# Optimization experiments

Measured on AMD Instinct MI355X. Metric: run time of the kernel, lower is better.

Reference implementation:

```python
import jax, jax.numpy as jnp
import numpy as np

N_USERS = 100_000
N_ITEMS = 200_000
EMBED_DIM = 64
N_LAYERS = 2
AVG_DEG = 32
BATCH = 8192


def setup_inputs() -> dict:
    rng = np.random.default_rng(0)
    n_inter = N_USERS * AVG_DEG
    u = rng.integers(0, N_USERS, n_inter).astype(np.int32)
    i = rng.integers(0, N_ITEMS, n_inter).astype(np.int32)
    # symmetric bipartite adjacency: (u, n_users+i) and (n_users+i, u)
    rows = np.concatenate([u, i + N_USERS]).astype(np.int32)
    cols = np.concatenate([i + N_USERS, u]).astype(np.int32)
    n_nodes = N_USERS + N_ITEMS
    deg = np.bincount(rows, minlength=n_nodes).astype(np.float32)
    d_inv = np.where(deg > 0, deg ** -0.5, 0.0).astype(np.float32)
    vals = (d_inv[rows] * d_inv[cols]).astype(np.float32)  # D^-1/2 A D^-1/2

    key = jax.random.key(0)
    k1, k2, k3, k4 = jax.random.split(key, 4)
    return {
        "users": jax.random.randint(k1, (BATCH,), 0, N_USERS, dtype=jnp.int32),
        "items": jax.random.randint(k2, (BATCH,), 0, N_ITEMS, dtype=jnp.int32),
        "user_emb": 0.1 * jax.random.normal(k3, (N_USERS, EMBED_DIM), dtype=jnp.float32),
        "item_emb": 0.1 * jax.random.normal(k4, (N_ITEMS, EMBED_DIM), dtype=jnp.float32),
        "rows": jnp.asarray(rows),
        "cols": jnp.asarray(cols),
        "vals": jnp.asarray(vals),
    }


def reference(users, items, user_emb, item_emb, rows, cols, vals):
    n_users = user_emb.shape[0]
    n_nodes = n_users + item_emb.shape[0]
    all_emb = jnp.concatenate([user_emb, item_emb], axis=0)  # [N, D]
    emb = all_emb
    acc = all_emb  # running sum over layer outputs (fused mean)
    for _ in range(N_LAYERS):
        # SpMM: out[r] += vals_e * emb[cols_e] for each edge e with row r
        emb = jax.ops.segment_sum(vals[:, None] * emb[cols], rows,
                                  num_segments=n_nodes)
        acc = acc + emb
    light_out = acc / jnp.float32(N_LAYERS + 1)  # mean over stacked layers
    users_emb = light_out[users]                    # [B, D]
    items_emb = light_out[n_users + items]          # [B, D]
    scores = jnp.sum(users_emb * items_emb, axis=1)  # [B]
    return users_emb, items_emb, scores
```

## Files before the change

### kernel.cpp

```cpp
#include <hip/hip_runtime.h>
#include <hip/hip_bf16.h>


#define DIM 64
#define BSH 8
#define BN 256
#define NBMAX 1184
#define T_PAIRS 6144
#define T_STAGE 12288
#define K3_THREADS 512
#define SCAP 10240

__global__ void build_bb(const int* __restrict__ users,
                         const int* __restrict__ items,
                         unsigned char* __restrict__ bb,
                         unsigned char* __restrict__ flag,
                         int batch, int n_users) {
    int t = blockIdx.x * blockDim.x + threadIdx.x;
    if (t >= 2 * batch) return;
    int node = (t < batch) ? users[t] : (n_users + items[t - batch]);
    bb[node] = 1;
    flag[node] = 1;
}

__global__ void count_reserve(const int* __restrict__ rows,
                              const int* __restrict__ cols,
                              int n_pairs, int nb,
                              int* __restrict__ gcnt,
                              int* __restrict__ rcnt, int* __restrict__ rbase) {
    __shared__ int cnt[NBMAX];
    int t = threadIdx.x;
    for (int b = t; b < nb; b += blockDim.x) cnt[b] = 0;
    __syncthreads();
    int e0 = blockIdx.x * T_PAIRS;
    int e1 = min(e0 + T_PAIRS, n_pairs);
    int n = e1 - e0;
    int n4 = n >> 2;
    const int4* r4 = (const int4*)(rows + e0);
    const int4* c4 = (const int4*)(cols + e0);
    for (int j = t; j < n4; j += blockDim.x) {
        int4 r = r4[j];
        int4 c = c4[j];
        atomicAdd(&cnt[r.x >> BSH], 1); atomicAdd(&cnt[c.x >> BSH], 1);
        atomicAdd(&cnt[r.y >> BSH], 1); atomicAdd(&cnt[c.y >> BSH], 1);
        atomicAdd(&cnt[r.z >> BSH], 1); atomicAdd(&cnt[c.z >> BSH], 1);
        atomicAdd(&cnt[r.w >> BSH], 1); atomicAdd(&cnt[c.w >> BSH], 1);
    }
    for (int i = e0 + (n4 << 2) + t; i < e1; i += blockDim.x) {
        atomicAdd(&cnt[rows[i] >> BSH], 1);
        atomicAdd(&cnt[cols[i] >> BSH], 1);
    }
    __syncthreads();
    size_t rbo = (size_t)blockIdx.x * nb;
    for (int b = t; b < nb; b += blockDim.x) {
        int v = cnt[b];
        rcnt[rbo + b] = v;
        rbase[rbo + b] = v ? atomicAdd(&gcnt[b], v) : 0;
    }
}

__global__ void scan_buckets(const int* __restrict__ gcnt, int* __restrict__ gbase,
                             int* __restrict__ offs, int nb, int n_nodes) {
    __shared__ int s[NBMAX + 1];
    int t = threadIdx.x;
    for (int b = t; b < nb; b += blockDim.x) s[b] = gcnt[b];
    __syncthreads();
    if (t == 0) {
        int run = 0;
        for (int b = 0; b < nb; ++b) { int v = s[b]; s[b] = run; run += v; }
        s[nb] = run;
    }
    __syncthreads();
    for (int b = t; b <= nb; b += blockDim.x) gbase[b] = s[b];
    if (t == 0) offs[n_nodes] = s[nb];
}

__global__ __launch_bounds__(K3_THREADS)
void tile_scatter(const int* __restrict__ rows, const int* __restrict__ cols,
                  const int* __restrict__ rcnt, const int* __restrict__ rbase,
                  const int* __restrict__ gbase, unsigned* __restrict__ barr,
                  int n_pairs, int nb) {
    __shared__ unsigned stage[T_STAGE];
    __shared__ int loff[NBMAX + 1];
    __shared__ int cur[NBMAX];
    __shared__ int rb2[NBMAX];
    __shared__ int wsum[8];
    int t = threadIdx.x;
    int lane = t & 63, wave = t >> 6;
    size_t rbo = (size_t)blockIdx.x * nb;

    int lo = t * 3;
    int c0 = (lo     < nb) ? rcnt[rbo + lo]     : 0;
    int c1 = (lo + 1 < nb) ? rcnt[rbo + lo + 1] : 0;
    int c2 = (lo + 2 < nb) ? rcnt[rbo + lo + 2] : 0;
    int s = c0 + c1 + c2;
    int x = s;
    #pragma unroll
    for (int o = 1; o < 64; o <<= 1) { int y = __shfl_up(x, o); if (lane >= o) x += y; }
    if (lane == 63) wsum[wave] = x;
    __syncthreads();
    int wb = 0;
    #pragma unroll
    for (int w = 0; w < 8; ++w) if (w < wave) wb += wsum[w];
    int run = wb + (x - s);
    if (lo < nb) {
        loff[lo] = run; cur[lo] = run;
        rb2[lo] = gbase[lo] + rbase[rbo + lo] - run;
    }
    if (lo + 1 < nb) {
        int r1 = run + c0;
        loff[lo + 1] = r1; cur[lo + 1] = r1;
        rb2[lo + 1] = gbase[lo + 1] + rbase[rbo + lo + 1] - r1;
    }
    if (lo + 2 < nb) {
        int r2 = run + c0 + c1;
        loff[lo + 2] = r2; cur[lo + 2] = r2;
        rb2[lo + 2] = gbase[lo + 2] + rbase[rbo + lo + 2] - r2;
    }
    int e0 = blockIdx.x * T_PAIRS;
    int e1 = min(e0 + T_PAIRS, n_pairs);
    int size = 2 * (e1 - e0);
    if (t == 0) loff[nb] = size;
    __syncthreads();

    {
        int n = e1 - e0;
        int n4 = n >> 2;
        const int4* r4 = (const int4*)(rows + e0);
        const int4* c4 = (const int4*)(cols + e0);
        for (int j = t; j < n4; j += K3_THREADS) {
            int4 r = r4[j];
            int4 c = c4[j];
            int u, v, b, p;
            u = r.x; v = c.x;
            b = u >> BSH; p = atomicAdd(&cur[b], 1);
            stage[p] = ((unsigned)(u & (BN - 1)) << 19) | (unsigned)v;
            b = v >> BSH; p = atomicAdd(&cur[b], 1);
            stage[p] = ((unsigned)(v & (BN - 1)) << 19) | (unsigned)u;
            u = r.y; v = c.y;
            b = u >> BSH; p = atomicAdd(&cur[b], 1);
            stage[p] = ((unsigned)(u & (BN - 1)) << 19) | (unsigned)v;
            b = v >> BSH; p = atomicAdd(&cur[b], 1);
            stage[p] = ((unsigned)(v & (BN - 1)) << 19) | (unsigned)u;
            u = r.z; v = c.z;
            b = u >> BSH; p = atomicAdd(&cur[b], 1);
            stage[p] = ((unsigned)(u & (BN - 1)) << 19) | (unsigned)v;
            b = v >> BSH; p = atomicAdd(&cur[b], 1);
            stage[p] = ((unsigned)(v & (BN - 1)) << 19) | (unsigned)u;
            u = r.w; v = c.w;
            b = u >> BSH; p = atomicAdd(&cur[b], 1);
            stage[p] = ((unsigned)(u & (BN - 1)) << 19) | (unsigned)v;
            b = v >> BSH; p = atomicAdd(&cur[b], 1);
            stage[p] = ((unsigned)(v & (BN - 1)) << 19) | (unsigned)u;
        }
        for (int i = e0 + (n4 << 2) + t; i < e1; i += K3_THREADS) {
            int u = rows[i];
            int v = cols[i];
            int b = u >> BSH;
            int p = atomicAdd(&cur[b], 1);
            stage[p] = ((unsigned)(u & (BN - 1)) << 19) | (unsigned)v;
            b = v >> BSH;
            p = atomicAdd(&cur[b], 1);
            stage[p] = ((unsigned)(v & (BN - 1)) << 19) | (unsigned)u;
        }
    }
    __syncthreads();

    int nchunks = (size + 15) >> 4;
    for (int c = t; c < nchunks; c += K3_THREADS) {
        int i0 = c << 4;
        int iend = min(i0 + 16, size);
        int l = 0, h = nb;
        while (h - l > 1) {
            int m = (l + h) >> 1;
            if (loff[m] <= i0) l = m; else h = m;
        }
        int b = l;
        int off = rb2[b];
        for (int i = i0; i < iend; ++i) {
            while (loff[b + 1] <= i) { ++b; off = rb2[b]; }
            barr[off + i] = stage[i];
        }
    }
}

__device__ __forceinline__ unsigned pack_bf16(float a, float b) {
    __hip_bfloat16 ha = __float2bfloat16(a);
    __hip_bfloat16 hb = __float2bfloat16(b);
    unsigned short ua, ub;
    __builtin_memcpy(&ua, &ha, 2);
    __builtin_memcpy(&ub, &hb, 2);
    return ((unsigned)ub << 16) | (unsigned)ua;
}

__global__ void node_sort(unsigned* __restrict__ barr, const int* __restrict__ gbase,
                          int* __restrict__ offs, float* __restrict__ d_inv,
                          const float* __restrict__ user_emb,
                          const float* __restrict__ item_emb,
                          unsigned* __restrict__ embs,
                          const unsigned char* __restrict__ bb,
                          unsigned char* __restrict__ flag,
                          int n_nodes, int n_users) {
    __shared__ unsigned stage[SCAP];
    __shared__ int cnt[BN];
    __shared__ int cur[BN];
    __shared__ float dinv_s[BN];
    int cb = blockIdx.x;
    int t = threadIdx.x;
    int nb0 = cb << BSH;
    int base = gbase[cb];
    int end  = gbase[cb + 1];
    int size = end - base; if (size > SCAP) size = SCAP;
    if (t < BN) cnt[t] = 0;
    __syncthreads();
    for (int i = t; i < size; i += blockDim.x) {
        unsigned e = barr[base + i];
        stage[i] = e;
        atomicAdd(&cnt[(int)(e >> 19)], 1);
    }
    __syncthreads();
    if (t < 64) {
        int j = t * 4;
        int c0 = cnt[j], c1 = cnt[j + 1], c2 = cnt[j + 2], c3 = cnt[j + 3];
        int s = c0 + c1 + c2 + c3;
        int x = s;
        #pragma unroll
        for (int o = 1; o < 64; o <<= 1) { int y = __shfl_up(x, o); if (t >= o) x += y; }
        int ex0 = x - s;
        int ex[4] = {ex0, ex0 + c0, ex0 + c0 + c1, ex0 + c0 + c1 + c2};
        int dg[4] = {c0, c1, c2, c3};
        cur[j] = ex[0]; cur[j + 1] = ex[1]; cur[j + 2] = ex[2]; cur[j + 3] = ex[3];
        #pragma unroll
        for (int k = 0; k < 4; ++k) {
            int node = nb0 + j + k;
            float di = dg[k] > 0 ? rsqrtf((float)dg[k]) : 0.0f;
            dinv_s[j + k] = di;
            if (node < n_nodes) {
                offs[node]  = base + ex[k];
                d_inv[node] = di;
            }
        }
    }
    __syncthreads();
    for (int i = t; i < size; i += blockDim.x) {
        unsigned e = stage[i];
        int p = atomicAdd(&cur[(int)(e >> 19)], 1);
        unsigned c = e & 0x7FFFFu;
        barr[base + p] = c;
        if (bb[nb0 + (int)(e >> 19)]) flag[c] = 1;
    }
    int q = t & 7;
    int nl0 = t >> 3;
    #pragma unroll
    for (int g = 0; g < 8; ++g) {
        int nl = nl0 + g * 32;
        int node = nb0 + nl;
        if (node >= n_nodes) break;
        float di = dinv_s[nl];
        const float* src = (node < n_users)
            ? (user_emb + (size_t)node * DIM)
            : (item_emb + (size_t)(node - n_users) * DIM);
        float4 f0 = *(const float4*)(src + q * 8);
        float4 f1 = *(const float4*)(src + q * 8 + 4);
        uint4 o;
        o.x = pack_bf16(di * f0.x, di * f0.y);
        o.y = pack_bf16(di * f0.z, di * f0.w);
        o.z = pack_bf16(di * f1.x, di * f1.y);
        o.w = pack_bf16(di * f1.z, di * f1.w);
        *(uint4*)(embs + (size_t)node * 32 + q * 4) = o;
    }
}

__device__ __forceinline__ float blo(unsigned g) { return __int_as_float(g << 16); }
__device__ __forceinline__ float bhi(unsigned g) { return __int_as_float(g & 0xFFFF0000u); }

__global__ void spmm_layer1(const int* __restrict__ offs,
                            const unsigned* __restrict__ csr,
                            const float* __restrict__ d_inv,
                            const unsigned* __restrict__ embs,
                            const unsigned char* __restrict__ flag,
                            float* __restrict__ z,
                            int n_nodes) {
    int wid = (blockIdx.x * blockDim.x + threadIdx.x) >> 6;
    int lane = threadIdx.x & 63;
    int half = lane >> 5;
    int row = wid * 2 + half;
    int l = lane & 31;
    int grp = l >> 3;
    int sub = l & 7;

    bool alive = (row < n_nodes) && flag[row];
    if (__ballot(alive) == 0ull) return;

    int start = 0, end = 0;
    if (alive) { start = offs[row]; end = offs[row + 1]; }

    float a0 = 0, a1 = 0, a2 = 0, a3 = 0, a4 = 0, a5 = 0, a6 = 0, a7 = 0;
    float b0 = 0, b1 = 0, b2 = 0, b3 = 0, b4 = 0, b5 = 0, b6 = 0, b7 = 0;
    int e = start;
    for (; e + 16 <= end; e += 16) {
        unsigned c0 = csr[e      + grp];
        unsigned c1 = csr[e + 4  + grp];
        unsigned c2 = csr[e + 8  + grp];
        unsigned c3 = csr[e + 12 + grp];
        uint4 g0 = *(const uint4*)(embs + (size_t)c0 * 32 + 4 * sub);
        uint4 g1 = *(const uint4*)(embs + (size_t)c1 * 32 + 4 * sub);
        uint4 g2 = *(const uint4*)(embs + (size_t)c2 * 32 + 4 * sub);
        uint4 g3 = *(const uint4*)(embs + (size_t)c3 * 32 + 4 * sub);
        a0 += blo(g0.x); a1 += bhi(g0.x); a2 += blo(g0.y); a3 += bhi(g0.y);
        a4 += blo(g0.z); a5 += bhi(g0.z); a6 += blo(g0.w); a7 += bhi(g0.w);
        b0 += blo(g1.x); b1 += bhi(g1.x); b2 += blo(g1.y); b3 += bhi(g1.y);
        b4 += blo(g1.z); b5 += bhi(g1.z); b6 += blo(g1.w); b7 += bhi(g1.w);
        a0 += blo(g2.x); a1 += bhi(g2.x); a2 += blo(g2.y); a3 += bhi(g2.y);
        a4 += blo(g2.z); a5 += bhi(g2.z); a6 += blo(g2.w); a7 += bhi(g2.w);
        b0 += blo(g3.x); b1 += bhi(g3.x); b2 += blo(g3.y); b3 += bhi(g3.y);
        b4 += blo(g3.z); b5 += bhi(g3.z); b6 += blo(g3.w); b7 += bhi(g3.w);
    }
    if (e < end) {
        int i0 = e      + grp;
        int i1 = e + 4  + grp;
        int i2 = e + 8  + grp;
        int i3 = e + 12 + grp;
        bool v0 = i0 < end, v1 = i1 < end, v2 = i2 < end, v3 = i3 < end;
        unsigned c0 = csr[v0 ? i0 : start];
        unsigned c1 = csr[v1 ? i1 : start];
        unsigned c2 = csr[v2 ? i2 : start];
        unsigned c3 = csr[v3 ? i3 : start];
        uint4 g0 = *(const uint4*)(embs + (size_t)c0 * 32 + 4 * sub);
        uint4 g1 = *(const uint4*)(embs + (size_t)c1 * 32 + 4 * sub);
        uint4 g2 = *(const uint4*)(embs + (size_t)c2 * 32 + 4 * sub);
        uint4 g3 = *(const uint4*)(embs + (size_t)c3 * 32 + 4 * sub);
        float m0 = v0 ? 1.0f : 0.0f;
        float m1 = v1 ? 1.0f : 0.0f;
        float m2 = v2 ? 1.0f : 0.0f;
        float m3 = v3 ? 1.0f : 0.0f;
        a0 += m0 * blo(g0.x); a1 += m0 * bhi(g0.x); a2 += m0 * blo(g0.y); a3 += m0 * bhi(g0.y);
        a4 += m0 * blo(g0.z); a5 += m0 * bhi(g0.z); a6 += m0 * blo(g0.w); a7 += m0 * bhi(g0.w);
        b0 += m1 * blo(g1.x); b1 += m1 * bhi(g1.x); b2 += m1 * blo(g1.y); b3 += m1 * bhi(g1.y);
        b4 += m1 * blo(g1.z); b5 += m1 * bhi(g1.z); b6 += m1 * blo(g1.w); b7 += m1 * bhi(g1.w);
        a0 += m2 * blo(g2.x); a1 += m2 * bhi(g2.x); a2 += m2 * blo(g2.y); a3 += m2 * bhi(g2.y);
        a4 += m2 * blo(g2.z); a5 += m2 * bhi(g2.z); a6 += m2 * blo(g2.w); a7 += m2 * bhi(g2.w);
        b0 += m3 * blo(g3.x); b1 += m3 * bhi(g3.x); b2 += m3 * blo(g3.y); b3 += m3 * bhi(g3.y);
        b4 += m3 * blo(g3.z); b5 += m3 * bhi(g3.z); b6 += m3 * blo(g3.w); b7 += m3 * bhi(g3.w);
    }
    a0 += b0; a1 += b1; a2 += b2; a3 += b3;
    a4 += b4; a5 += b5; a6 += b6; a7 += b7;
    a0 += __shfl_down(a0, 16); a1 += __shfl_down(a1, 16);
    a2 += __shfl_down(a2, 16); a3 += __shfl_down(a3, 16);
    a4 += __shfl_down(a4, 16); a5 += __shfl_down(a5, 16);
    a6 += __shfl_down(a6, 16); a7 += __shfl_down(a7, 16);
    a0 += __shfl_down(a0, 8);  a1 += __shfl_down(a1, 8);
    a2 += __shfl_down(a2, 8);  a3 += __shfl_down(a3, 8);
    a4 += __shfl_down(a4, 8);  a5 += __shfl_down(a5, 8);
    a6 += __shfl_down(a6, 8);  a7 += __shfl_down(a7, 8);
    if (alive && l < 8) {
        float di = d_inv[row];
        float w = di * di;
        float4 o0; o0.x = a0 * w; o0.y = a1 * w; o0.z = a2 * w; o0.w = a3 * w;
        float4 o1; o1.x = a4 * w; o1.y = a5 * w; o1.z = a6 * w; o1.w = a7 * w;
        *(float4*)(z + (size_t)row * DIM + 8 * sub)     = o0;
        *(float4*)(z + (size_t)row * DIM + 8 * sub + 4) = o1;
    }
}

__device__ __forceinline__ void gatherz2(const int* __restrict__ offs,
                                         const unsigned* __restrict__ csr,
                                         const float* __restrict__ z,
                                         int nodeA, int nodeB, int lane,
                                         float& rA, float& rB) {
    int sa = offs[nodeA], ea = offs[nodeA + 1];
    int sb = offs[nodeB], eb = offs[nodeB + 1];
    float a0 = 0, a1 = 0, a2 = 0, a3 = 0;
    float b0 = 0, b1 = 0, b2 = 0, b3 = 0;
    int na = ea - sa, nbn = eb - sb;
    int mx = na > nbn ? na : nbn;
    for (int k = 0; k < mx; k += 4) {
        int ia = sa + k, ib = sb + k;
        unsigned cA0 = csr[ia     < ea ? ia     : 0];
        unsigned cA1 = csr[ia + 1 < ea ? ia + 1 : 0];
        unsigned cA2 = csr[ia + 2 < ea ? ia + 2 : 0];
        unsigned cA3 = csr[ia + 3 < ea ? ia + 3 : 0];
        unsigned cB0 = csr[ib     < eb ? ib     : 0];
        unsigned cB1 = csr[ib + 1 < eb ? ib + 1 : 0];
        unsigned cB2 = csr[ib + 2 < eb ? ib + 2 : 0];
        unsigned cB3 = csr[ib + 3 < eb ? ib + 3 : 0];
        float zA0 = z[(size_t)cA0 * DIM + lane];
        float zA1 = z[(size_t)cA1 * DIM + lane];
        float zA2 = z[(size_t)cA2 * DIM + lane];
        float zA3 = z[(size_t)cA3 * DIM + lane];
        float zB0 = z[(size_t)cB0 * DIM + lane];
        float zB1 = z[(size_t)cB1 * DIM + lane];
        float zB2 = z[(size_t)cB2 * DIM + lane];
        float zB3 = z[(size_t)cB3 * DIM + lane];
        a0 += (ia     < ea) ? zA0 : 0.0f;
        a1 += (ia + 1 < ea) ? zA1 : 0.0f;
        a2 += (ia + 2 < ea) ? zA2 : 0.0f;
        a3 += (ia + 3 < ea) ? zA3 : 0.0f;
        b0 += (ib     < eb) ? zB0 : 0.0f;
        b1 += (ib + 1 < eb) ? zB1 : 0.0f;
        b2 += (ib + 2 < eb) ? zB2 : 0.0f;
        b3 += (ib + 3 < eb) ? zB3 : 0.0f;
    }
    rA = (a0 + a1) + (a2 + a3);
    rB = (b0 + b1) + (b2 + b3);
}

__global__ void epilogue_kernel(const int* __restrict__ users,
                                const int* __restrict__ items,
                                const float* __restrict__ user_emb,
                                const float* __restrict__ item_emb,
                                const float* __restrict__ z,
                                const int* __restrict__ offs,
                                const unsigned* __restrict__ csr,
                                const float* __restrict__ d_inv,
                                float* __restrict__ out_u,
                                float* __restrict__ out_i,
                                float* __restrict__ out_s,
                                int batch, int n_users) {
    int w = (blockIdx.x * blockDim.x + threadIdx.x) >> 6;
    int lane = threadIdx.x & 63;
    if (w >= batch) return;
    int u  = users[w];
    int it = items[w];
    int ni = n_users + it;

    float du = d_inv[u], dn = d_inv[ni];
    float gu, gi;
    gatherz2(offs, csr, z, u, ni, lane, gu, gi);
    float ue2 = du * gu;
    float ie2 = dn * gi;

    float e1u = (du > 0.0f) ? z[(size_t)u  * DIM + lane] / du : 0.0f;
    float e1i = (dn > 0.0f) ? z[(size_t)ni * DIM + lane] / dn : 0.0f;

    const float inv3 = 1.0f / 3.0f;
    float ue = (user_emb[(size_t)u  * DIM + lane] + e1u + ue2) * inv3;
    float ie = (item_emb[(size_t)it * DIM + lane] + e1i + ie2) * inv3;

    out_u[(size_t)w * DIM + lane] = ue;
    out_i[(size_t)w * DIM + lane] = ie;

    float s = ue * ie;
    #pragma unroll
    for (int o = 32; o > 0; o >>= 1) s += __shfl_down(s, o);
    if (lane == 0) out_s[w] = s;
}

extern "C" void kernel_launch(void* const* d_in, const int* in_sizes, int n_in,
                              void* d_out, int out_size, void* d_ws, size_t ws_size,
                              hipStream_t stream) {
    const int*   users    = (const int*)d_in[0];
    const int*   items    = (const int*)d_in[1];
    const float* user_emb = (const float*)d_in[2];
    const float* item_emb = (const float*)d_in[3];
    const int*   rows     = (const int*)d_in[4];
    const int*   cols     = (const int*)d_in[5];

    const int batch   = in_sizes[0];
    const int n_users = in_sizes[2] / DIM;
    const int n_items = in_sizes[3] / DIM;
    const int n_nodes = n_users + n_items;
    const int n_edges = in_sizes[4];
    const int n_pairs = n_edges / 2;

    const int nb      = (n_nodes + BN - 1) >> BSH;
    const int n_tiles = (n_pairs + T_PAIRS - 1) / T_PAIRS;

    char* p = (char*)d_ws;
    float*    z     = (float*)p;    p += (size_t)n_nodes * DIM * sizeof(float);
    int*      offs  = (int*)p;      p += (size_t)(n_nodes + 1) * sizeof(int);
    float*    d_inv = (float*)p;    p += (size_t)n_nodes * sizeof(float);
    int*      gcnt  = (int*)p;      p += (size_t)nb * sizeof(int);
    int*      gbase = (int*)p;      p += (size_t)(nb + 1) * sizeof(int);
    int*      rcnt  = (int*)p;      p += (size_t)n_tiles * nb * sizeof(int);
    int*      rbase = (int*)p;      p += (size_t)n_tiles * nb * sizeof(int);
    unsigned* barr  = (unsigned*)p; p += (size_t)n_edges * sizeof(unsigned);
    unsigned* embs  = (unsigned*)p; p += (size_t)n_nodes * 32 * sizeof(unsigned);
    unsigned char* bb   = (unsigned char*)p; p += (size_t)n_nodes;
    unsigned char* flag = (unsigned char*)p; p += (size_t)n_nodes;

    float* out_u = (float*)d_out;
    float* out_i = out_u + (size_t)batch * DIM;
    float* out_s = out_i + (size_t)batch * DIM;

    hipMemsetAsync(gcnt, 0, (size_t)nb * sizeof(int), stream);
    hipMemsetAsync(bb, 0, 2 * (size_t)n_nodes, stream);
    build_bb<<<(2 * batch + 255) / 256, 256, 0, stream>>>(users, items, bb, flag,
                                                          batch, n_users);
    count_reserve<<<n_tiles, 256, 0, stream>>>(rows, cols, n_pairs, nb,
                                               gcnt, rcnt, rbase);
    scan_buckets<<<1, 256, 0, stream>>>(gcnt, gbase, offs, nb, n_nodes);
    tile_scatter<<<n_tiles, K3_THREADS, 0, stream>>>(rows, cols, rcnt, rbase,
                                                     gbase, barr, n_pairs, nb);
    node_sort<<<nb, 256, 0, stream>>>(barr, gbase, offs, d_inv,
                                      user_emb, item_emb, embs,
                                      bb, flag, n_nodes, n_users);

    spmm_layer1<<<(n_nodes + 7) / 8, 256, 0, stream>>>(offs, barr, d_inv,
                                                       embs, flag, z, n_nodes);
    epilogue_kernel<<<(batch + 3) / 4, 256, 0, stream>>>(users, items,
                                                         user_emb, item_emb, z,
                                                         offs, barr, d_inv,
                                                         out_u, out_i, out_s,
                                                         batch, n_users);
}
```

Measured before the change: 475.1 us.

## Replace tiled bucket-sort CSR build with per-node degree count and atomic scatter

Drops the two-level bucket sort (per-tile counts, shared-memory staging, per-bucket node sort) used to build the CSR adjacency. The new version counts per-node degrees with global atomics, derives bucket sums and offsets from those counts, then scatters each edge straight to its slot through per-node atomic cursors. The two-hop neighbour flags are now set in a separate kernel that walks the adjacency lists of the batch nodes. This cuts kernel count and shared-memory staging, but it relies on heavy global atomics with random access and leaves edge order within a row nondeterministic.

```diff
diff --git a/kernel.cpp b/kernel.cpp
--- a/kernel.cpp
+++ b/kernel.cpp
@@ -6,57 +6,50 @@
 #define BSH 8
 #define BN 256
 #define NBMAX 1184
-#define T_PAIRS 6144
-#define T_STAGE 12288
-#define K3_THREADS 512
-#define SCAP 10240
-
-__global__ void build_bb(const int* __restrict__ users,
-                         const int* __restrict__ items,
-                         unsigned char* __restrict__ bb,
-                         unsigned char* __restrict__ flag,
-                         int batch, int n_users) {
+
+__global__ void build_flag(const int* __restrict__ users,
+                           const int* __restrict__ items,
+                           unsigned char* __restrict__ flag,
+                           int batch, int n_users) {
     int t = blockIdx.x * blockDim.x + threadIdx.x;
     if (t >= 2 * batch) return;
     int node = (t < batch) ? users[t] : (n_users + items[t - batch]);
-    bb[node] = 1;
     flag[node] = 1;
 }
 
-__global__ void count_reserve(const int* __restrict__ rows,
-                              const int* __restrict__ cols,
-                              int n_pairs, int nb,
-                              int* __restrict__ gcnt,
-                              int* __restrict__ rcnt, int* __restrict__ rbase) {
-    __shared__ int cnt[NBMAX];
+__global__ void deg_count(const int* __restrict__ rows,
+                          const int* __restrict__ cols,
+                          int n_pairs, int* __restrict__ deg) {
+    int idx = blockIdx.x * blockDim.x + threadIdx.x;
+    int i4 = n_pairs >> 2;
+    if (idx < i4) {
+        int4 r = ((const int4*)rows)[idx];
+        int4 c = ((const int4*)cols)[idx];
+        atomicAdd(&deg[r.x], 1); atomicAdd(&deg[c.x], 1);
+        atomicAdd(&deg[r.y], 1); atomicAdd(&deg[c.y], 1);
+        atomicAdd(&deg[r.z], 1); atomicAdd(&deg[c.z], 1);
+        atomicAdd(&deg[r.w], 1); atomicAdd(&deg[c.w], 1);
+    }
+    int tail0 = i4 << 2;
+    int rem = n_pairs - tail0;
+    if (idx < rem) {
+        atomicAdd(&deg[rows[tail0 + idx]], 1);
+        atomicAdd(&deg[cols[tail0 + idx]], 1);
+    }
+}
+
+__global__ void bucket_sum(const int* __restrict__ deg,
+                           int* __restrict__ gcnt, int n_nodes) {
+    __shared__ int red[4];
+    int b = blockIdx.x;
     int t = threadIdx.x;
-    for (int b = t; b < nb; b += blockDim.x) cnt[b] = 0;
+    int node = (b << BSH) + t;
+    int v = (node < n_nodes) ? deg[node] : 0;
+    #pragma unroll
+    for (int o = 32; o > 0; o >>= 1) v += __shfl_down(v, o);
+    if ((t & 63) == 0) red[t >> 6] = v;
     __syncthreads();
-    int e0 = blockIdx.x * T_PAIRS;
-    int e1 = min(e0 + T_PAIRS, n_pairs);
-    int n = e1 - e0;
-    int n4 = n >> 2;
-    const int4* r4 = (const int4*)(rows + e0);
-    const int4* c4 = (const int4*)(cols + e0);
-    for (int j = t; j < n4; j += blockDim.x) {
-        int4 r = r4[j];
-        int4 c = c4[j];
-        atomicAdd(&cnt[r.x >> BSH], 1); atomicAdd(&cnt[c.x >> BSH], 1);
-        atomicAdd(&cnt[r.y >> BSH], 1); atomicAdd(&cnt[c.y >> BSH], 1);
-        atomicAdd(&cnt[r.z >> BSH], 1); atomicAdd(&cnt[c.z >> BSH], 1);
-        atomicAdd(&cnt[r.w >> BSH], 1); atomicAdd(&cnt[c.w >> BSH], 1);
-    }
-    for (int i = e0 + (n4 << 2) + t; i < e1; i += blockDim.x) {
-        atomicAdd(&cnt[rows[i] >> BSH], 1);
-        atomicAdd(&cnt[cols[i] >> BSH], 1);
-    }
-    __syncthreads();
-    size_t rbo = (size_t)blockIdx.x * nb;
-    for (int b = t; b < nb; b += blockDim.x) {
-        int v = cnt[b];
-        rcnt[rbo + b] = v;
-        rbase[rbo + b] = v ? atomicAdd(&gcnt[b], v) : 0;
-    }
+    if (t == 0) gcnt[b] = red[0] + red[1] + red[2] + red[3];
 }
 
 __global__ void scan_buckets(const int* __restrict__ gcnt, int* __restrict__ gbase,
@@ -75,115 +68,6 @@
     if (t == 0) offs[n_nodes] = s[nb];
 }
 
-__global__ __launch_bounds__(K3_THREADS)
-void tile_scatter(const int* __restrict__ rows, const int* __restrict__ cols,
-                  const int* __restrict__ rcnt, const int* __restrict__ rbase,
-                  const int* __restrict__ gbase, unsigned* __restrict__ barr,
-                  int n_pairs, int nb) {
-    __shared__ unsigned stage[T_STAGE];
-    __shared__ int loff[NBMAX + 1];
-    __shared__ int cur[NBMAX];
-    __shared__ int rb2[NBMAX];
-    __shared__ int wsum[8];
-    int t = threadIdx.x;
-    int lane = t & 63, wave = t >> 6;
-    size_t rbo = (size_t)blockIdx.x * nb;
-
-    int lo = t * 3;
-    int c0 = (lo     < nb) ? rcnt[rbo + lo]     : 0;
-    int c1 = (lo + 1 < nb) ? rcnt[rbo + lo + 1] : 0;
-    int c2 = (lo + 2 < nb) ? rcnt[rbo + lo + 2] : 0;
-    int s = c0 + c1 + c2;
-    int x = s;
-    #pragma unroll
-    for (int o = 1; o < 64; o <<= 1) { int y = __shfl_up(x, o); if (lane >= o) x += y; }
-    if (lane == 63) wsum[wave] = x;
-    __syncthreads();
-    int wb = 0;
-    #pragma unroll
-    for (int w = 0; w < 8; ++w) if (w < wave) wb += wsum[w];
-    int run = wb + (x - s);
-    if (lo < nb) {
-        loff[lo] = run; cur[lo] = run;
-        rb2[lo] = gbase[lo] + rbase[rbo + lo] - run;
-    }
-    if (lo + 1 < nb) {
-        int r1 = run + c0;
-        loff[lo + 1] = r1; cur[lo + 1] = r1;
-        rb2[lo + 1] = gbase[lo + 1] + rbase[rbo + lo + 1] - r1;
-    }
-    if (lo + 2 < nb) {
-        int r2 = run + c0 + c1;
-        loff[lo + 2] = r2; cur[lo + 2] = r2;
-        rb2[lo + 2] = gbase[lo + 2] + rbase[rbo + lo + 2] - r2;
-    }
-    int e0 = blockIdx.x * T_PAIRS;
-    int e1 = min(e0 + T_PAIRS, n_pairs);
-    int size = 2 * (e1 - e0);
-    if (t == 0) loff[nb] = size;
-    __syncthreads();
-
-    {
-        int n = e1 - e0;
-        int n4 = n >> 2;
-        const int4* r4 = (const int4*)(rows + e0);
-        const int4* c4 = (const int4*)(cols + e0);
-        for (int j = t; j < n4; j += K3_THREADS) {
-            int4 r = r4[j];
-            int4 c = c4[j];
-            int u, v, b, p;
-            u = r.x; v = c.x;
-            b = u >> BSH; p = atomicAdd(&cur[b], 1);
-            stage[p] = ((unsigned)(u & (BN - 1)) << 19) | (unsigned)v;
-            b = v >> BSH; p = atomicAdd(&cur[b], 1);
-            stage[p] = ((unsigned)(v & (BN - 1)) << 19) | (unsigned)u;
-            u = r.y; v = c.y;
-            b = u >> BSH; p = atomicAdd(&cur[b], 1);
-            stage[p] = ((unsigned)(u & (BN - 1)) << 19) | (unsigned)v;
-            b = v >> BSH; p = atomicAdd(&cur[b], 1);
-            stage[p] = ((unsigned)(v & (BN - 1)) << 19) | (unsigned)u;
-            u = r.z; v = c.z;
-            b = u >> BSH; p = atomicAdd(&cur[b], 1);
-            stage[p] = ((unsigned)(u & (BN - 1)) << 19) | (unsigned)v;
-            b = v >> BSH; p = atomicAdd(&cur[b], 1);
-            stage[p] = ((unsigned)(v & (BN - 1)) << 19) | (unsigned)u;
-            u = r.w; v = c.w;
-            b = u >> BSH; p = atomicAdd(&cur[b], 1);
-            stage[p] = ((unsigned)(u & (BN - 1)) << 19) | (unsigned)v;
-            b = v >> BSH; p = atomicAdd(&cur[b], 1);
-            stage[p] = ((unsigned)(v & (BN - 1)) << 19) | (unsigned)u;
-        }
-        for (int i = e0 + (n4 << 2) + t; i < e1; i += K3_THREADS) {
-            int u = rows[i];
-            int v = cols[i];
-            int b = u >> BSH;
-            int p = atomicAdd(&cur[b], 1);
-            stage[p] = ((unsigned)(u & (BN - 1)) << 19) | (unsigned)v;
-            b = v >> BSH;
-            p = atomicAdd(&cur[b], 1);
-            stage[p] = ((unsigned)(v & (BN - 1)) << 19) | (unsigned)u;
-        }
-    }
-    __syncthreads();
-
-    int nchunks = (size + 15) >> 4;
-    for (int c = t; c < nchunks; c += K3_THREADS) {
-        int i0 = c << 4;
-        int iend = min(i0 + 16, size);
-        int l = 0, h = nb;
-        while (h - l > 1) {
-            int m = (l + h) >> 1;
-            if (loff[m] <= i0) l = m; else h = m;
-        }
-        int b = l;
-        int off = rb2[b];
-        for (int i = i0; i < iend; ++i) {
-            while (loff[b + 1] <= i) { ++b; off = rb2[b]; }
-            barr[off + i] = stage[i];
-        }
-    }
-}
-
 __device__ __forceinline__ unsigned pack_bf16(float a, float b) {
     __hip_bfloat16 ha = __float2bfloat16(a);
     __hip_bfloat16 hb = __float2bfloat16(b);
@@ -193,82 +77,103 @@
     return ((unsigned)ub << 16) | (unsigned)ua;
 }
 
-__global__ void node_sort(unsigned* __restrict__ barr, const int* __restrict__ gbase,
-                          int* __restrict__ offs, float* __restrict__ d_inv,
-                          const float* __restrict__ user_emb,
-                          const float* __restrict__ item_emb,
-                          unsigned* __restrict__ embs,
-                          const unsigned char* __restrict__ bb,
-                          unsigned char* __restrict__ flag,
-                          int n_nodes, int n_users) {
-    __shared__ unsigned stage[SCAP];
-    __shared__ int cnt[BN];
-    __shared__ int cur[BN];
+__global__ void expand_prescale(const int* __restrict__ deg,
+                                const int* __restrict__ gbase,
+                                int* __restrict__ offs, int* __restrict__ cursor,
+                                float* __restrict__ d_inv,
+                                const float* __restrict__ user_emb,
+                                const float* __restrict__ item_emb,
+                                unsigned* __restrict__ embs,
+                                int n_nodes, int n_users) {
+    __shared__ int wsum[4];
     __shared__ float dinv_s[BN];
-    int cb = blockIdx.x;
+    int b = blockIdx.x;
     int t = threadIdx.x;
-    int nb0 = cb << BSH;
-    int base = gbase[cb];
-    int end  = gbase[cb + 1];
-    int size = end - base; if (size > SCAP) size = SCAP;
-    if (t < BN) cnt[t] = 0;
+    int lane = t & 63, wave = t >> 6;
+    int node = (b << BSH) + t;
+    int d = (node < n_nodes) ? deg[node] : 0;
+    int x = d;
+    #pragma unroll
+    for (int o = 1; o < 64; o <<= 1) { int y = __shfl_up(x, o); if (lane >= o) x += y; }
+    if (lane == 63) wsum[wave] = x;
     __syncthreads();
-    for (int i = t; i < size; i += blockDim.x) {
-        unsigned e = barr[base + i];
-        stage[i] = e;
-        atomicAdd(&cnt[(int)(e >> 19)], 1);
+    int wb = 0;
+    #pragma unroll
+    for (int w = 0; w < 4; ++w) if (w < wave) wb += wsum[w];
+    int ex = wb + x - d;
+    float di = (d > 0) ? rsqrtf((float)d) : 0.0f;
+    dinv_s[t] = di;
+    int base = gbase[b];
+    if (node < n_nodes) {
+        offs[node]   = base + ex;
+        cursor[node] = base + ex;
+        d_inv[node]  = di;
     }
     __syncthreads();
-    if (t < 64) {
-        int j = t * 4;
-        int c0 = cnt[j], c1 = cnt[j + 1], c2 = cnt[j + 2], c3 = cnt[j + 3];
-        int s = c0 + c1 + c2 + c3;
-        int x = s;
-        #pragma unroll
-        for (int o = 1; o < 64; o <<= 1) { int y = __shfl_up(x, o); if (t >= o) x += y; }
-        int ex0 = x - s;
-        int ex[4] = {ex0, ex0 + c0, ex0 + c0 + c1, ex0 + c0 + c1 + c2};
-        int dg[4] = {c0, c1, c2, c3};
-        cur[j] = ex[0]; cur[j + 1] = ex[1]; cur[j + 2] = ex[2]; cur[j + 3] = ex[3];
-        #pragma unroll
-        for (int k = 0; k < 4; ++k) {
-            int node = nb0 + j + k;
-            float di = dg[k] > 0 ? rsqrtf((float)dg[k]) : 0.0f;
-            dinv_s[j + k] = di;
-            if (node < n_nodes) {
-                offs[node]  = base + ex[k];
-                d_inv[node] = di;
-            }
-        }
-    }
-    __syncthreads();
-    for (int i = t; i < size; i += blockDim.x) {
-        unsigned e = stage[i];
-        int p = atomicAdd(&cur[(int)(e >> 19)], 1);
-        unsigned c = e & 0x7FFFFu;
-        barr[base + p] = c;
-        if (bb[nb0 + (int)(e >> 19)]) flag[c] = 1;
-    }
     int q = t & 7;
     int nl0 = t >> 3;
     #pragma unroll
     for (int g = 0; g < 8; ++g) {
         int nl = nl0 + g * 32;
-        int node = nb0 + nl;
-        if (node >= n_nodes) break;
-        float di = dinv_s[nl];
-        const float* src = (node < n_users)
-            ? (user_emb + (size_t)node * DIM)
-            : (item_emb + (size_t)(node - n_users) * DIM);
+        int nd = (b << BSH) + nl;
+        if (nd >= n_nodes) break;
+        float dv = dinv_s[nl];
+        const float* src = (nd < n_users)
+            ? (user_emb + (size_t)nd * DIM)
+            : (item_emb + (size_t)(nd - n_users) * DIM);
         float4 f0 = *(const float4*)(src + q * 8);
         float4 f1 = *(const float4*)(src + q * 8 + 4);
         uint4 o;
-        o.x = pack_bf16(di * f0.x, di * f0.y);
-        o.y = pack_bf16(di * f0.z, di * f0.w);
-        o.z = pack_bf16(di * f1.x, di * f1.y);
-        o.w = pack_bf16(di * f1.z, di * f1.w);
-        *(uint4*)(embs + (size_t)node * 32 + q * 4) = o;
-    }
+        o.x = pack_bf16(dv * f0.x, dv * f0.y);
+        o.y = pack_bf16(dv * f0.z, dv * f0.w);
+        o.z = pack_bf16(dv * f1.x, dv * f1.y);
+        o.w = pack_bf16(dv * f1.z, dv * f1.w);
+        *(uint4*)(embs + (size_t)nd * 32 + q * 4) = o;
+    }
+}
+
+__global__ void scatter_edges(const int* __restrict__ rows,
+                              const int* __restrict__ cols,
+                              int n_pairs,
+                              int* __restrict__ cursor,
+                              unsigned* __restrict__ barr) {
+    int idx = blockIdx.x * blockDim.x + threadIdx.x;
+    int i4 = n_pairs >> 2;
+    if (idx < i4) {
+        int4 r = ((const int4*)rows)[idx];
+        int4 c = ((const int4*)cols)[idx];
+        int p;
+        p = atomicAdd(&cursor[r.x], 1); barr[p] = (unsigned)c.x;
+        p = atomicAdd(&cursor[c.x], 1); barr[p] = (unsigned)r.x;
+        p = atomicAdd(&cursor[r.y], 1); barr[p] = (unsigned)c.y;
+        p = atomicAdd(&cursor[c.y], 1); barr[p] = (unsigned)r.y;
+        p = atomicAdd(&cursor[r.z], 1); barr[p] = (unsigned)c.z;
+        p = atomicAdd(&cursor[c.z], 1); barr[p] = (unsigned)r.z;
+        p = atomicAdd(&cursor[r.w], 1); barr[p] = (unsigned)c.w;
+        p = atomicAdd(&cursor[c.w], 1); barr[p] = (unsigned)r.w;
+    }
+    int tail0 = i4 << 2;
+    int rem = n_pairs - tail0;
+    if (idx < rem) {
+        int u = rows[tail0 + idx];
+        int v = cols[tail0 + idx];
+        int p = atomicAdd(&cursor[u], 1); barr[p] = (unsigned)v;
+        p = atomicAdd(&cursor[v], 1); barr[p] = (unsigned)u;
+    }
+}
+
+__global__ void flag_neighbors(const int* __restrict__ users,
+                               const int* __restrict__ items,
+                               const int* __restrict__ offs,
+                               const unsigned* __restrict__ barr,
+                               unsigned char* __restrict__ flag,
+                               int batch, int n_users) {
+    int w = (blockIdx.x * blockDim.x + threadIdx.x) >> 6;
+    int lane = threadIdx.x & 63;
+    if (w >= 2 * batch) return;
+    int node = (w < batch) ? users[w] : (n_users + items[w - batch]);
+    int s = offs[node], e = offs[node + 1];
+    for (int i = s + lane; i < e; i += 64) flag[barr[i]] = 1;
 }
 
 __device__ __forceinline__ float blo(unsigned g) { return __int_as_float(g << 16); }
@@ -463,38 +368,40 @@
     const int n_edges = in_sizes[4];
     const int n_pairs = n_edges / 2;
 
-    const int nb      = (n_nodes + BN - 1) >> BSH;
-    const int n_tiles = (n_pairs + T_PAIRS - 1) / T_PAIRS;
+    const int nb = (n_nodes + BN - 1) >> BSH;
 
     char* p = (char*)d_ws;
     float*    z     = (float*)p;    p += (size_t)n_nodes * DIM * sizeof(float);
+    unsigned* embs  = (unsigned*)p; p += (size_t)n_nodes * 32 * sizeof(unsigned);
     int*      offs  = (int*)p;      p += (size_t)(n_nodes + 1) * sizeof(int);
     float*    d_inv = (float*)p;    p += (size_t)n_nodes * sizeof(float);
+    int*      gbase = (int*)p;      p += (size_t)(nb + 1) * sizeof(int);
+    int*      cursor= (int*)p;      p += (size_t)n_nodes * sizeof(int);
+    unsigned* barr  = (unsigned*)p; p += (size_t)n_edges * sizeof(unsigned);
+    int*      deg   = (int*)p;      p += (size_t)n_nodes * sizeof(int);
     int*      gcnt  = (int*)p;      p += (size_t)nb * sizeof(int);
-    int*      gbase = (int*)p;      p += (size_t)(nb + 1) * sizeof(int);
-    int*      rcnt  = (int*)p;      p += (size_t)n_tiles * nb * sizeof(int);
-    int*      rbase = (int*)p;      p += (size_t)n_tiles * nb * sizeof(int);
-    unsigned* barr  = (unsigned*)p; p += (size_t)n_edges * sizeof(unsigned);
-    unsigned* embs  = (unsigned*)p; p += (size_t)n_nodes * 32 * sizeof(unsigned);
-    unsigned char* bb   = (unsigned char*)p; p += (size_t)n_nodes;
     unsigned char* flag = (unsigned char*)p; p += (size_t)n_nodes;
+    size_t zero_bytes = (size_t)n_nodes * sizeof(int) + (size_t)nb * sizeof(int)
+                      + (size_t)n_nodes;
 
     float* out_u = (float*)d_out;
     float* out_i = out_u + (size_t)batch * DIM;
     float* out_s = out_i + (size_t)batch * DIM;
 
-    hipMemsetAsync(gcnt, 0, (size_t)nb * sizeof(int), stream);
-    hipMemsetAsync(bb, 0, 2 * (size_t)n_nodes, stream);
-    build_bb<<<(2 * batch + 255) / 256, 256, 0, stream>>>(users, items, bb, flag,
-                                                          batch, n_users);
-    count_reserve<<<n_tiles, 256, 0, stream>>>(rows, cols, n_pairs, nb,
-                                               gcnt, rcnt, rbase);
+    hipMemsetAsync(deg, 0, zero_bytes, stream);
+    build_flag<<<(2 * batch + 255) / 256, 256, 0, stream>>>(users, items, flag,
+                                                            batch, n_users);
+    const int i4 = n_pairs >> 2;
+    const int egrid = (i4 + 255) / 256 > 0 ? (i4 + 255) / 256 : 1;
+    deg_count<<<egrid, 256, 0, stream>>>(rows, cols, n_pairs, deg);
+    bucket_sum<<<nb, 256, 0, stream>>>(deg, gcnt, n_nodes);
     scan_buckets<<<1, 256, 0, stream>>>(gcnt, gbase, offs, nb, n_nodes);
-    tile_scatter<<<n_tiles, K3_THREADS, 0, stream>>>(rows, cols, rcnt, rbase,
-                                                     gbase, barr, n_pairs, nb);
-    node_sort<<<nb, 256, 0, stream>>>(barr, gbase, offs, d_inv,
-                                      user_emb, item_emb, embs,
-                                      bb, flag, n_nodes, n_users);
+    expand_prescale<<<nb, 256, 0, stream>>>(deg, gbase, offs, cursor, d_inv,
+                                            user_emb, item_emb, embs,
+                                            n_nodes, n_users);
+    scatter_edges<<<egrid, 256, 0, stream>>>(rows, cols, n_pairs, cursor, barr);
+    flag_neighbors<<<(2 * batch * 64 + 255) / 256, 256, 0, stream>>>(
+        users, items, offs, barr, flag, batch, n_users);
 
     spmm_layer1<<<(n_nodes + 7) / 8, 256, 0, stream>>>(offs, barr, d_inv,
                                                        embs, flag, z, n_nodes);
```

Measured after the change: 1.131 ms. +138.0%, slower.
